# Performance work log

Hardware: AMD Instinct MI355X
Metric: run time of the kernel (lower is better)

## Reference

```python
import jax, jax.numpy as jnp
import numpy as np

N, D_IN, D_H, D_ATT, C_CLUST, N_CLS = 10000, 1024, 512, 256, 10, 4


def setup_inputs() -> dict:
    key = jax.random.key(0)
    ks = jax.random.split(key, 20)
    s = 0.02
    return {
        "x": jax.random.normal(ks[0], (N, D_IN), dtype=jnp.float32),
        "cluster_id": jax.random.randint(ks[1], (N,), 0, C_CLUST, dtype=jnp.int64),
        # per-cluster phi: Linear(1024->512) + ReLU + Linear(512->512) + ReLU
        "W1": s * jax.random.normal(ks[2], (C_CLUST, D_IN, D_H), dtype=jnp.float32),
        "b1": jnp.zeros((C_CLUST, D_H), dtype=jnp.float32),
        "W2": s * jax.random.normal(ks[3], (C_CLUST, D_H, D_H), dtype=jnp.float32),
        "b2": jnp.zeros((C_CLUST, D_H), dtype=jnp.float32),
        # attention_net fc: Linear(512->512)+ReLU
        "Wfc": s * jax.random.normal(ks[4], (D_H, D_H), dtype=jnp.float32),
        "bfc": jnp.zeros((D_H,), dtype=jnp.float32),
        # Attn_Net_Gated
        "Wa": s * jax.random.normal(ks[5], (D_H, D_ATT), dtype=jnp.float32),
        "ba": jnp.zeros((D_ATT,), dtype=jnp.float32),
        "Wb": s * jax.random.normal(ks[6], (D_H, D_ATT), dtype=jnp.float32),
        "bb": jnp.zeros((D_ATT,), dtype=jnp.float32),
        "Wc": s * jax.random.normal(ks[7], (D_ATT, 1), dtype=jnp.float32),
        "bc": jnp.zeros((1,), dtype=jnp.float32),
        # rho: Linear(512->256)+ReLU
        "Wr": s * jax.random.normal(ks[8], (D_H, D_ATT), dtype=jnp.float32),
        "br": jnp.zeros((D_ATT,), dtype=jnp.float32),
        # classifier: Linear(256->4)
        "Wcls": s * jax.random.normal(ks[9], (D_ATT, N_CLS), dtype=jnp.float32),
        "bcls": jnp.zeros((N_CLS,), dtype=jnp.float32),
    }


def reference(x, cluster_id, W1, b1, W2, b2, Wfc, bfc, Wa, ba, Wb, bb, Wc, bc, Wr, br, Wcls, bcls):
    C = W1.shape[0]
    # dense dispatch: apply every cluster's phi, then masked-mean per cluster
    # (ReLU is per-point elementwise, so masked mean == mean over members)
    h1 = jax.nn.relu(jnp.einsum('nd,cdh->cnh', x, W1) + b1[:, None, :])   # [C,N,512]
    h2 = jax.nn.relu(jnp.einsum('cnh,chk->cnk', h1, W2) + b2[:, None, :]) # [C,N,512]
    mask = (cluster_id[None, :] == jnp.arange(C)[:, None]).astype(h2.dtype)  # [C,N]
    counts = jnp.maximum(mask.sum(axis=1), 1.0)                           # [C]
    pooled = jnp.einsum('cnk,cn->ck', h2, mask) / counts[:, None]         # [C,512]
    # attention_net: fc + gated attention
    h = jax.nn.relu(pooled @ Wfc + bfc)                                   # [C,512]
    gate = jnp.tanh(h @ Wa + ba) * jax.nn.sigmoid(h @ Wb + bb)            # [C,256]
    A = (gate @ Wc + bc)                                                  # [C,1]
    A = jax.nn.softmax(A.T, axis=1)                                       # [1,C]
    h_path = A @ h                                                        # [1,512]
    hr = jax.nn.relu(h_path @ Wr + br)                                    # [1,256]
    logits = (hr[0] @ Wcls + bcls)[None, :]                               # [1,4]
    Y_prob = jax.nn.softmax(logits, axis=1)
    Y_hat = jnp.argmax(logits, axis=1)[:, None]
    return logits, Y_prob, Y_hat
```

## Files before the change

kernel.cpp:

```cpp
#include <hip/hip_runtime.h>
#include <math.h>

#define DIN 1024
#define DH 512
#define DATT 256
#define CNUM 10
#define NCLS 4
#define NH 64
#define NSC 40

typedef __attribute__((ext_vector_type(8))) short bf16x8;
typedef __attribute__((ext_vector_type(4))) float f32x4;
typedef unsigned short ushort_t;
typedef unsigned int uint_t;

__device__ inline ushort_t f2bf(float f) {
    uint_t u = __float_as_uint(f);
    u += 0x7FFF + ((u >> 16) & 1);
    return (ushort_t)(u >> 16);
}

__device__ inline void gl_lds16(const void* g, void* l) {
    __builtin_amdgcn_global_load_lds(
        (const __attribute__((address_space(1))) unsigned int*)g,
        (__attribute__((address_space(3))) unsigned int*)l, 16, 0, 0);
}


__global__ __launch_bounds__(256) void k_prep(
    const int* __restrict__ cid, int n, const float* __restrict__ bc,
    const float* __restrict__ x, const float* __restrict__ W1, const float* __restrict__ W2,
    ushort_t* __restrict__ xb, ushort_t* __restrict__ W1t, ushort_t* __restrict__ W2t,
    int nxb, int nw,
    float* __restrict__ a_logit, int* __restrict__ scat_pos, int* __restrict__ bucket)
{
    int bid = blockIdx.x;
    int t = threadIdx.x;

    if (bid == 0) {
        if (t < CNUM) a_logit[t] = bc[0];
        return;
    }
    bid -= 1;

    if (bid < NSC) {
        int lane = t & 63;
        for (int i = bid * 256 + t; i < n; i += NSC * 256) {
            int c = cid[i];
            #pragma unroll
            for (int cc = 0; cc < CNUM; cc++) {
                unsigned long long mask = __ballot(c == cc);
                if (mask == 0ull) continue;
                int leader = __ffsll(mask) - 1;
                int basep = 0;
                if (lane == leader) basep = atomicAdd(&scat_pos[cc], __popcll(mask));
                basep = __shfl(basep, leader, 64);
                if (c == cc) {
                    int rank = __popcll(mask & ((1ull << lane) - 1ull));
                    bucket[cc * n + basep + rank] = i;
                }
            }
        }
        return;
    }
    bid -= NSC;

    if (bid < nxb) {
        int row = bid * 4 + (t >> 6);
        if (row >= n) return;
        int col = (t & 63) * 16;
        const float* src = x + (size_t)row * DIN + col;
        ushort_t* dst = xb + (size_t)row * DIN + col;
        #pragma unroll
        for (int j = 0; j < 4; j++) {
            float4 v = *(const float4*)(src + 4 * j);
            *(ushort4*)(dst + 4 * j) = make_ushort4(f2bf(v.x), f2bf(v.y), f2bf(v.z), f2bf(v.w));
        }
        return;
    }
    bid -= nxb;

    if (bid < nw) {
        __shared__ float tile[64][65];
        int z = bid >> 7;
        int kx = (bid & 127) >> 3;
        int ny = bid & 7;
        const float* src; ushort_t* dst; int K;
        if (z < CNUM) { K = DIN; src = W1 + (size_t)z * K * DH; dst = W1t + (size_t)z * DH * K; }
        else          { K = DH;  src = W2 + (size_t)(z - CNUM) * K * DH; dst = W2t + (size_t)(z - CNUM) * DH * K; }
        int k0 = kx * 64;
        if (k0 >= K) return;
        int n0 = ny * 64;
        int rr = t >> 4;
        int cc = (t & 15) * 4;
        #pragma unroll
        for (int i = 0; i < 4; i++) {
            int row = rr + 16 * i;
            float4 v = *(const float4*)(src + (size_t)(k0 + row) * DH + n0 + cc);
            tile[row][cc + 0] = v.x; tile[row][cc + 1] = v.y;
            tile[row][cc + 2] = v.z; tile[row][cc + 3] = v.w;
        }
        __syncthreads();
        #pragma unroll
        for (int i = 0; i < 4; i++) {
            int nrow = rr + 16 * i;
            ushort4 o = make_ushort4(f2bf(tile[cc + 0][nrow]), f2bf(tile[cc + 1][nrow]),
                                     f2bf(tile[cc + 2][nrow]), f2bf(tile[cc + 3][nrow]));
            *(ushort4*)(dst + (size_t)(n0 + nrow) * K + k0 + cc) = o;
        }
    }
}


__device__ inline void stage4(
    const ushort_t* a0, const ushort_t* a1,
    const ushort_t* b0, const ushort_t* b1,
    int ko, ushort_t* As, ushort_t* Bs, int t)
{
    gl_lds16(a0 + ko, As + 0 * 2048 + t * 8);
    gl_lds16(a1 + ko, As + 1 * 2048 + t * 8);
    gl_lds16(b0 + ko, Bs + 0 * 2048 + t * 8);
    gl_lds16(b1 + ko, Bs + 1 * 2048 + t * 8);
}

__device__ inline void mfma_tile64(const ushort_t* As, const ushort_t* Bs,
                                   f32x4 (&acc)[2][2], int wr, int wc, int m, int quad)
{
    bf16x8 a[2][2], b[2][2];
    #pragma unroll
    for (int ks = 0; ks < 2; ks++) {
        int chunk = ((ks * 4 + quad) ^ (m & 7)) * 8;
        #pragma unroll
        for (int mf = 0; mf < 2; mf++)
            a[ks][mf] = *(const bf16x8*)(As + (32 * wr + 16 * mf + m) * 64 + chunk);
        #pragma unroll
        for (int nf = 0; nf < 2; nf++)
            b[ks][nf] = *(const bf16x8*)(Bs + (32 * wc + 16 * nf + m) * 64 + chunk);
    }
    asm volatile("s_waitcnt lgkmcnt(0)" ::: "memory");
    __builtin_amdgcn_sched_barrier(0);
    __builtin_amdgcn_s_barrier();
    __builtin_amdgcn_sched_barrier(0);
    #pragma unroll
    for (int ks = 0; ks < 2; ks++)
        #pragma unroll
        for (int mf = 0; mf < 2; mf++)
            #pragma unroll
            for (int nf = 0; nf < 2; nf++)
                acc[mf][nf] = __builtin_amdgcn_mfma_f32_16x16x32_bf16(a[ks][mf], b[ks][nf], acc[mf][nf], 0, 0, 0);
}

__device__ inline void gemm_loop64(
    const ushort_t* a0, const ushort_t* a1,
    const ushort_t* b0, const ushort_t* b1,
    int KT, f32x4 (&acc)[2][2], ushort_t* As, ushort_t* Bs)
{
    int t = threadIdx.x;
    int lane = t & 63;
    int w = t >> 6, wr = w >> 1, wc = w & 1;
    int m = lane & 15, quad = lane >> 4;

    stage4(a0, a1, b0, b1, 0, As, Bs, t);
    for (int kt = 0; kt < KT; kt += 2) {
        stage4(a0, a1, b0, b1, (kt + 1) * 64, As + 4096, Bs + 4096, t);
        asm volatile("s_waitcnt vmcnt(4)" ::: "memory");
        __builtin_amdgcn_sched_barrier(0);
        __builtin_amdgcn_s_barrier();
        __builtin_amdgcn_sched_barrier(0);
        mfma_tile64(As, Bs, acc, wr, wc, m, quad);

        if (kt + 2 < KT) {
            stage4(a0, a1, b0, b1, (kt + 2) * 64, As, Bs, t);
            asm volatile("s_waitcnt vmcnt(4)" ::: "memory");
        } else {
            asm volatile("s_waitcnt vmcnt(0)" ::: "memory");
        }
        __builtin_amdgcn_sched_barrier(0);
        __builtin_amdgcn_s_barrier();
        __builtin_amdgcn_sched_barrier(0);
        mfma_tile64(As + 4096, Bs + 4096, acc, wr, wc, m, quad);
    }
}

__device__ inline int tile_decode(int bid, int MAXT, const int* counts,
                                  int& c, int& m0, int& tile_n)
{
    int mt, nt;
    if ((MAXT & 7) == 0) {
        int mtpx = MAXT >> 3;
        int xcd = bid & 7, j = bid >> 3;
        nt = j / mtpx;
        mt = xcd * mtpx + (j - nt * mtpx);
    } else { mt = bid >> 3; nt = bid & 7; }

    int rem = mt;
    c = 0;
    #pragma unroll
    for (int cc = 0; cc < CNUM; cc++) {
        int tc = (counts[cc] + 63) >> 6;
        if (rem < tc) { c = cc; m0 = rem * 64; tile_n = nt * 64; return 1; }
        rem -= tc;
    }
    return 0;
}

__global__ __launch_bounds__(256, 4) void k_g1(
    const ushort_t* __restrict__ xb, const ushort_t* __restrict__ W1t,
    const float* __restrict__ b1, const int* __restrict__ bucket,
    const int* __restrict__ counts, int n, int MAXT,
    ushort_t* __restrict__ H1)
{
    __shared__ ushort_t As[2][64][64];
    __shared__ ushort_t Bs[2][64][64];

    int c, m0, tile_n;
    if (!tile_decode(blockIdx.x, MAXT, counts, c, m0, tile_n)) return;
    int cnt = counts[c];

    int t = threadIdx.x;
    int rr = t >> 3;
    int swz = ((t & 7) ^ (rr & 7)) * 8;

    const ushort_t* aP[2];
    const ushort_t* bP[2];
    #pragma unroll
    for (int s = 0; s < 2; s++) {
        int ra = m0 + s * 32 + rr;
        if (ra > cnt - 1) ra = cnt - 1;
        aP[s] = xb + (size_t)bucket[c * n + ra] * DIN + swz;
        bP[s] = W1t + ((size_t)c * DH + tile_n + s * 32 + rr) * DIN + swz;
    }

    f32x4 acc[2][2] = {};
    gemm_loop64(aP[0], aP[1], bP[0], bP[1], DIN / 64, acc, &As[0][0][0], &Bs[0][0][0]);

    int lane = t & 63;
    int w = t >> 6, wr = w >> 1, wc = w & 1;
    int m = lane & 15, quad = lane >> 4;
    int col0 = tile_n + 32 * wc;
    #pragma unroll
    for (int nf = 0; nf < 2; nf++) {
        int col = col0 + 16 * nf + m;
        float bv = b1[c * DH + col];
        #pragma unroll
        for (int mf = 0; mf < 2; mf++) {
            int rowb = m0 + 32 * wr + 16 * mf + quad * 4;
            #pragma unroll
            for (int r = 0; r < 4; r++) {
                int row = rowb + r;
                if (row < cnt)
                    H1[((size_t)c * n + row) * DH + col] = f2bf(fmaxf(acc[mf][nf][r] + bv, 0.f));
            }
        }
    }
}

__global__ __launch_bounds__(256, 4) void k_g2(
    const ushort_t* __restrict__ H1, const ushort_t* __restrict__ W2t,
    const float* __restrict__ b2, const int* __restrict__ counts, int n, int MAXT,
    float* __restrict__ pooled)
{
    __shared__ ushort_t As[2][64][64];
    __shared__ ushort_t Bs[2][64][64];

    int c, m0, tile_n;
    if (!tile_decode(blockIdx.x, MAXT, counts, c, m0, tile_n)) return;
    int cnt = counts[c];

    int t = threadIdx.x;
    int rr = t >> 3;
    int swz = ((t & 7) ^ (rr & 7)) * 8;

    const ushort_t* aP[2];
    const ushort_t* bP[2];
    #pragma unroll
    for (int s = 0; s < 2; s++) {
        int ra = m0 + s * 32 + rr;
        if (ra > cnt - 1) ra = cnt - 1;
        aP[s] = H1 + ((size_t)c * n + ra) * DH + swz;
        bP[s] = W2t + ((size_t)c * DH + tile_n + s * 32 + rr) * DH + swz;
    }

    f32x4 acc[2][2] = {};
    gemm_loop64(aP[0], aP[1], bP[0], bP[1], DH / 64, acc, &As[0][0][0], &Bs[0][0][0]);

    int lane = t & 63;
    int w = t >> 6, wr = w >> 1, wc = w & 1;
    int m = lane & 15, quad = lane >> 4;
    int col0 = tile_n + 32 * wc;
    #pragma unroll
    for (int nf = 0; nf < 2; nf++) {
        int col = col0 + 16 * nf + m;
        float bv = b2[c * DH + col];
        float s = 0.f;
        #pragma unroll
        for (int mf = 0; mf < 2; mf++) {
            int rowb = m0 + 32 * wr + 16 * mf + quad * 4;
            #pragma unroll
            for (int r = 0; r < 4; r++) {
                int row = rowb + r;
                if (row < cnt) s += fmaxf(acc[mf][nf][r] + bv, 0.f);
            }
        }
        s += __shfl_xor(s, 16);
        s += __shfl_xor(s, 32);
        if (quad == 0) atomicAdd(&pooled[c * DH + col], s);
    }
}


__global__ __launch_bounds__(256) void k_fc2(
    const float* __restrict__ pooled, const int* __restrict__ counts,
    const float* __restrict__ Wfc, const float* __restrict__ bfc,
    float* __restrict__ hfc)
{
    int c = blockIdx.x;
    int c0 = blockIdx.y * 64;
    __shared__ float ps[DH];
    __shared__ float red[4][64];
    int t = threadIdx.x;
    float cnt = fmaxf((float)counts[c], 1.f);
    ps[t] = pooled[c * DH + t] / cnt;
    ps[t + 256] = pooled[c * DH + t + 256] / cnt;
    __syncthreads();
    int col = c0 + (t & 63);
    int ks = t >> 6;
    float acc = 0.f;
    #pragma unroll 8
    for (int k = ks * 128; k < ks * 128 + 128; k++)
        acc = fmaf(ps[k], Wfc[(size_t)k * DH + col], acc);
    red[ks][t & 63] = acc;
    __syncthreads();
    if (t < 64) {
        float v = red[0][t] + red[1][t] + red[2][t] + red[3][t] + bfc[c0 + t];
        hfc[c * DH + c0 + t] = fmaxf(v, 0.f);
    }
}

__global__ __launch_bounds__(256) void k_gate2(
    const float* __restrict__ hfc,
    const float* __restrict__ Wa, const float* __restrict__ ba,
    const float* __restrict__ Wb, const float* __restrict__ bb,
    const float* __restrict__ Wc,
    float* __restrict__ a_logit)
{
    int c = blockIdx.x;
    int d0 = blockIdx.y * 64;
    __shared__ float hf[DH];
    __shared__ float ra[4][64], rb[4][64];
    int t = threadIdx.x;
    hf[t] = hfc[c * DH + t];
    hf[t + 256] = hfc[c * DH + t + 256];
    __syncthreads();
    int d = d0 + (t & 63);
    int ks = t >> 6;
    float ga = 0.f, gb = 0.f;
    #pragma unroll 8
    for (int k = ks * 128; k < ks * 128 + 128; k++) {
        float h = hf[k];
        ga = fmaf(h, Wa[(size_t)k * DATT + d], ga);
        gb = fmaf(h, Wb[(size_t)k * DATT + d], gb);
    }
    ra[ks][t & 63] = ga;
    rb[ks][t & 63] = gb;
    __syncthreads();
    if (t < 64) {
        float sa = ra[0][t] + ra[1][t] + ra[2][t] + ra[3][t] + ba[d0 + t];
        float sb = rb[0][t] + rb[1][t] + rb[2][t] + rb[3][t] + bb[d0 + t];
        float g = tanhf(sa) * (1.f / (1.f + expf(-sb)));
        float p = g * Wc[d0 + t];
        #pragma unroll
        for (int off = 32; off >= 1; off >>= 1) p += __shfl_down(p, off, 64);
        if (t == 0) atomicAdd(&a_logit[c], p);
    }
}

__global__ __launch_bounds__(1024) void k_final(
    const float* __restrict__ hfc, const float* __restrict__ a_logit,
    const float* __restrict__ Wr, const float* __restrict__ br,
    const float* __restrict__ Wcls, const float* __restrict__ bcls,
    float* __restrict__ out)
{
    int t = threadIdx.x;
    __shared__ float hp[DH];
    __shared__ float r1[4][DATT];
    __shared__ float hr[DATT];
    __shared__ float wred[4][NCLS];

    float al[CNUM];
    float m = -1e30f;
    #pragma unroll
    for (int c = 0; c < CNUM; c++) { al[c] = a_logit[c]; m = fmaxf(m, al[c]); }
    float s = 0.f;
    #pragma unroll
    for (int c = 0; c < CNUM; c++) { al[c] = expf(al[c] - m); s += al[c]; }
    float inv = 1.f / s;

    if (t < DH) {
        float v = 0.f;
        #pragma unroll
        for (int c = 0; c < CNUM; c++) v = fmaf(al[c] * inv, hfc[c * DH + t], v);
        hp[t] = v;
    }
    __syncthreads();

    int d = t & 255;
    int ks = t >> 8;
    float acc = 0.f;
    #pragma unroll 8
    for (int k = ks * 128; k < ks * 128 + 128; k++)
        acc = fmaf(hp[k], Wr[(size_t)k * DATT + d], acc);
    r1[ks][d] = acc;
    __syncthreads();
    if (t < DATT)
        hr[t] = fmaxf(r1[0][t] + r1[1][t] + r1[2][t] + r1[3][t] + br[t], 0.f);
    __syncthreads();

    if (t < 256) {
        float h = hr[t];
        #pragma unroll
        for (int cls = 0; cls < NCLS; cls++) {
            float p = h * Wcls[(size_t)t * NCLS + cls];
            #pragma unroll
            for (int off = 32; off >= 1; off >>= 1) p += __shfl_down(p, off, 64);
            if ((t & 63) == 0) wred[t >> 6][cls] = p;
        }
    }
// ... 44 lines not shown
            }
        }
        __syncthreads();
        if (t < CNUM) counts_part[bid * 16 + t] = h[t];
        return;
    }

    for (int i = t; i < CNUM * DH; i += 256) pooled[i] = 0.f;
    if (t < CNUM) a_logit[t] = bc[0];
    if (t < CNUM) scat_pos[t] = 0;
}

__global__ __launch_bounds__(256) void k_scat_fb(
    const int* __restrict__ cid, int n, const int* __restrict__ counts_part,
    int* __restrict__ counts, int* __restrict__ offsets,
    int* __restrict__ scat_pos, int* __restrict__ bucket)
{
    int bid = blockIdx.x;
    int t = threadIdx.x;
    __shared__ int cnts[CNUM], off[CNUM];
    if (t < CNUM) {
        int s = 0;
        #pragma unroll 8
        for (int b = 0; b < NH; b++) s += counts_part[b * 16 + t];
        cnts[t] = s;
    }
    __syncthreads();
    if (t == 0) {
        int a = 0;
        for (int c = 0; c < CNUM; c++) { off[c] = a; a += cnts[c]; }
        if (bid == 0) {
            int aa = 0;
            for (int c = 0; c < CNUM; c++) { offsets[c] = aa; counts[c] = cnts[c]; aa += cnts[c]; }
            offsets[CNUM] = aa;
        }
    }
    __syncthreads();
    int lane = t & 63;
    for (int i = bid * 256 + t; i < n; i += NSC * 256) {
        int c = cid[i];
        #pragma unroll
        for (int cc = 0; cc < CNUM; cc++) {
            unsigned long long mask = __ballot(c == cc);
            if (mask == 0ull) continue;
            int leader = __ffsll(mask) - 1;
            int basep = 0;
            if (lane == leader) basep = atomicAdd(&scat_pos[cc], __popcll(mask));
            basep = __shfl(basep, leader, 64);
            if (c == cc) {
                int rank = __popcll(mask & ((1ull << lane) - 1ull));
                bucket[off[cc] + basep + rank] = i;
            }
        }
    }
}

#define MT 64
#define NT 128
#define KT 32

__global__ __launch_bounds__(256) void k_gemm1(
    const float* __restrict__ x, const float* __restrict__ W1, const float* __restrict__ b1,
    const int* __restrict__ bucket, const int* __restrict__ offsets, const int* __restrict__ counts,
    float* __restrict__ H1)
{
    int c = blockIdx.z;
    int cnt = counts[c];
    int m0 = blockIdx.x * MT;
    if (m0 >= cnt) return;
    int rows = min(MT, cnt - m0);
    int n0 = blockIdx.y * NT;
    int base = offsets[c];

    __shared__ float As[KT][MT + 4];
    __shared__ float Bs[KT][NT];

    int t = threadIdx.x;
    int tr = t >> 4;
    int tc = t & 15;
    int lr = t >> 2;
    int lk = (t & 3) * 8;
    const float* xrow = nullptr;
    if (lr < rows) xrow = x + (size_t)bucket[base + m0 + lr] * DIN;

    float acc[4][8];
    #pragma unroll
    for (int i = 0; i < 4; i++)
        #pragma unroll
        for (int j = 0; j < 8; j++) acc[i][j] = 0.f;

    const float* Wp = W1 + (size_t)c * DIN * DH + n0;

    for (int k0 = 0; k0 < DIN; k0 += KT) {
        __syncthreads();
        if (xrow) {
            float4 v0 = *(const float4*)(xrow + k0 + lk);
            float4 v1 = *(const float4*)(xrow + k0 + lk + 4);
            As[lk + 0][lr] = v0.x; As[lk + 1][lr] = v0.y;
            As[lk + 2][lr] = v0.z; As[lk + 3][lr] = v0.w;
            As[lk + 4][lr] = v1.x; As[lk + 5][lr] = v1.y;
            As[lk + 6][lr] = v1.z; As[lk + 7][lr] = v1.w;
        } else {
            #pragma unroll
            for (int i = 0; i < 8; i++) As[lk + i][lr] = 0.f;
        }
        #pragma unroll
// ... 111 lines not shown
        float s = 0.f;
        #pragma unroll
        for (int i = 0; i < 4; i++) {
            if (4 * tr + i < rows) s += fmaxf(acc[i][j] + bias, 0.f);
        }
        red[tr][cidx] = s;
    }
    __syncthreads();
    if (t < NT) {
        float s = 0.f;
        #pragma unroll
        for (int r = 0; r < 16; r++) s += red[r][t];
        atomicAdd(&pooled[c * DH + n0 + t], s);
    }
}


extern "C" void kernel_launch(void* const* d_in, const int* in_sizes, int n_in,
                              void* d_out, int out_size, void* d_ws, size_t ws_size,
                              hipStream_t stream) {
    (void)n_in; (void)out_size;
    const float* x    = (const float*)d_in[0];
    const int*   cid  = (const int*)d_in[1];
    const float* W1   = (const float*)d_in[2];
    const float* b1   = (const float*)d_in[3];
    const float* W2   = (const float*)d_in[4];
    const float* b2   = (const float*)d_in[5];
    const float* Wfc  = (const float*)d_in[6];
    const float* bfc  = (const float*)d_in[7];
    const float* Wa   = (const float*)d_in[8];
    const float* ba   = (const float*)d_in[9];
    const float* Wb   = (const float*)d_in[10];
    const float* bb   = (const float*)d_in[11];
    const float* Wc   = (const float*)d_in[12];
    const float* bc   = (const float*)d_in[13];
    const float* Wr   = (const float*)d_in[14];
    const float* br   = (const float*)d_in[15];
    const float* Wcls = (const float*)d_in[16];
    const float* bcls = (const float*)d_in[17];
    float* out = (float*)d_out;
    float* ws  = (float*)d_ws;

    int n = in_sizes[1];

    float* pooled   = ws;
    int*   scat_pos = (int*)(ws + 5120);
    float* a_logit  = ws + 5136;
    float* hfc      = ws + 5152;
    int*   bucket   = (int*)(ws + 10272);

    size_t big0 = (((size_t)(10272 + (size_t)CNUM * n) * 4) + 255) & ~(size_t)255;
    size_t w1t_bytes = (size_t)CNUM * DH * DIN * 2;
    size_t w2t_bytes = (size_t)CNUM * DH * DH * 2;
    size_t h1_bytes  = (size_t)CNUM * n * DH * 2;
    size_t xb_bytes  = (size_t)n * DIN * 2;
    size_t need = big0 + w1t_bytes + w2t_bytes + h1_bytes + xb_bytes;

    if (ws_size >= need) {
        ushort_t* W1t = (ushort_t*)((char*)d_ws + big0);
        ushort_t* W2t = (ushort_t*)((char*)d_ws + big0 + w1t_bytes);
        ushort_t* H1  = (ushort_t*)((char*)d_ws + big0 + w1t_bytes + w2t_bytes);
        ushort_t* xb  = (ushort_t*)((char*)d_ws + big0 + w1t_bytes + w2t_bytes + h1_bytes);

        int nxb = (n + 3) / 4;
        int nw  = 128 * 2 * CNUM;
        int MAXT = ((n / 64 + CNUM + 1) + 7) & ~7;

        hipMemsetAsync(ws, 0, 5136 * 4, stream);
        k_prep<<<1 + NSC + nxb + nw, 256, 0, stream>>>(
            cid, n, bc, x, W1, W2, xb, W1t, W2t, nxb, nw, a_logit, scat_pos, bucket);
        k_g1<<<8 * MAXT, 256, 0, stream>>>(xb, W1t, b1, bucket, scat_pos, n, MAXT, H1);
        k_g2<<<8 * MAXT, 256, 0, stream>>>(H1, W2t, b2, scat_pos, n, MAXT, pooled);
        k_fc2<<<dim3(CNUM, 8), 256, 0, stream>>>(pooled, scat_pos, Wfc, bfc, hfc);
        k_gate2<<<dim3(CNUM, 4), 256, 0, stream>>>(hfc, Wa, ba, Wb, bb, Wc, a_logit);
        k_final<<<1, 1024, 0, stream>>>(hfc, a_logit, Wr, br, Wcls, bcls, out);
    } else {
        float* pooledF     = ws + 0;
        int*   countsF     = (int*)(ws + 5120);
        int*   offsetsF    = (int*)(ws + 5136);
        float* a_logitF    = ws + 5168;
        int*   scat_posF   = (int*)(ws + 5184);
        float* hfcF        = ws + 5200;
        int*   counts_part = (int*)(ws + 10320);
        int*   bucketF     = (int*)(ws + 11344);

        k_hist<<<NH + 1, 256, 0, stream>>>(cid, n, bc, counts_part, pooledF, a_logitF, scat_posF);
        k_scat_fb<<<NSC, 256, 0, stream>>>(cid, n, counts_part, countsF, offsetsF, scat_posF, bucketF);

        float* H1f = ws + ((11344 + n + 31) & ~31);
        dim3 gg((n + MT - 1) / MT, DH / NT, CNUM);
        k_gemm1<<<gg, 256, 0, stream>>>(x, W1, b1, bucketF, offsetsF, countsF, H1f);
        k_gemm2<<<gg, 256, 0, stream>>>(H1f, W2, b2, offsetsF, countsF, pooledF);

        k_fc2<<<dim3(CNUM, 8), 256, 0, stream>>>(pooledF, countsF, Wfc, bfc, hfcF);
        k_gate2<<<dim3(CNUM, 4), 256, 0, stream>>>(hfcF, Wa, ba, Wb, bb, Wc, a_logitF);
        k_final<<<1, 1024, 0, stream>>>(hfcF, a_logitF, Wr, br, Wcls, bcls, out);
    }
}
```

Baseline: 221.7 us.

## Fuse x bf16 conversion into GEMM1 A-load and merge head kernels

Removes the separate pass that converts x to bf16. The first grouped GEMM now reads the fp32 rows of x gathered through the bucket, converts them in registers with packed bf16 converts and writes them to LDS, while W1 still streams through global-to-LDS loads. The fc and gated-attention kernels are merged into one 512-thread kernel per cluster that computes the attention logit directly, so the atomic and the bc initialisation go away. In exchange, GEMM1 fetches fp32 A data at twice the bytes, once per N tile (8 times per row), and uses a simpler double-buffered pipeline with extra barriers. The merged head kernel also runs fewer blocks.

Result: slower. 284.5 us (+28.4%).

```diff
diff --git a/kernel.cpp b/kernel.cpp
--- a/kernel.cpp
+++ b/kernel.cpp
@@ -20,6 +20,12 @@
     return (ushort_t)(u >> 16);
 }
 
+__device__ inline uint_t pkbf(float lo, float hi) {
+    uint_t r;
+    asm("v_cvt_pk_bf16_f32 %0, %1, %2" : "=v"(r) : "v"(lo), "v"(hi));
+    return r;
+}
+
 __device__ inline void gl_lds16(const void* g, void* l) {
     __builtin_amdgcn_global_load_lds(
         (const __attribute__((address_space(1))) unsigned int*)g,
@@ -28,20 +34,14 @@
 
 
 __global__ __launch_bounds__(256) void k_prep(
-    const int* __restrict__ cid, int n, const float* __restrict__ bc,
-    const float* __restrict__ x, const float* __restrict__ W1, const float* __restrict__ W2,
-    ushort_t* __restrict__ xb, ushort_t* __restrict__ W1t, ushort_t* __restrict__ W2t,
-    int nxb, int nw,
-    float* __restrict__ a_logit, int* __restrict__ scat_pos, int* __restrict__ bucket)
+    const int* __restrict__ cid, int n,
+    const float* __restrict__ W1, const float* __restrict__ W2,
+    ushort_t* __restrict__ W1t, ushort_t* __restrict__ W2t,
+    int nw,
+    int* __restrict__ scat_pos, int* __restrict__ bucket)
 {
     int bid = blockIdx.x;
     int t = threadIdx.x;
-
-    if (bid == 0) {
-        if (t < CNUM) a_logit[t] = bc[0];
-        return;
-    }
-    bid -= 1;
 
     if (bid < NSC) {
         int lane = t & 63;
@@ -64,21 +64,6 @@
         return;
     }
     bid -= NSC;
-
-    if (bid < nxb) {
-        int row = bid * 4 + (t >> 6);
-        if (row >= n) return;
-        int col = (t & 63) * 16;
-        const float* src = x + (size_t)row * DIN + col;
-        ushort_t* dst = xb + (size_t)row * DIN + col;
-        #pragma unroll
-        for (int j = 0; j < 4; j++) {
-            float4 v = *(const float4*)(src + 4 * j);
-            *(ushort4*)(dst + 4 * j) = make_ushort4(f2bf(v.x), f2bf(v.y), f2bf(v.z), f2bf(v.w));
-        }
-        return;
-    }
-    bid -= nxb;
 
     if (bid < nw) {
         __shared__ float tile[64][65];
@@ -112,6 +97,150 @@
 }
 
 
+__device__ inline void awrite(ushort_t* A, int o0, int o1,
+                              const float4& r0, const float4& r1,
+                              const float4& r2, const float4& r3)
+{
+    uint4 w0, w1;
+    w0.x = pkbf(r0.x, r0.y); w0.y = pkbf(r0.z, r0.w);
+    w0.z = pkbf(r1.x, r1.y); w0.w = pkbf(r1.z, r1.w);
+    w1.x = pkbf(r2.x, r2.y); w1.y = pkbf(r2.z, r2.w);
+    w1.z = pkbf(r3.x, r3.y); w1.w = pkbf(r3.z, r3.w);
+    *(uint4*)(A + o0) = w0;
+    *(uint4*)(A + o1) = w1;
+}
+
+__device__ inline int tile_decode(int bid, int MAXT, const int* counts,
+                                  int& c, int& m0, int& tile_n)
+{
+    int mt, nt;
+    if ((MAXT & 7) == 0) {
+        int mtpx = MAXT >> 3;
+        int xcd = bid & 7, j = bid >> 3;
+        nt = j / mtpx;
+        mt = xcd * mtpx + (j - nt * mtpx);
+    } else { mt = bid >> 3; nt = bid & 7; }
+
+    int rem = mt;
+    c = 0;
+    #pragma unroll
+    for (int cc = 0; cc < CNUM; cc++) {
+        int tc = (counts[cc] + 63) >> 6;
+        if (rem < tc) { c = cc; m0 = rem * 64; tile_n = nt * 64; return 1; }
+        rem -= tc;
+    }
+    return 0;
+}
+
+
+__global__ __launch_bounds__(256, 4) void k_g1(
+    const float* __restrict__ x, const ushort_t* __restrict__ W1t,
+    const float* __restrict__ b1, const int* __restrict__ bucket,
+    const int* __restrict__ counts, int n, int MAXT,
+    ushort_t* __restrict__ H1)
+{
+    __shared__ ushort_t As[2][64][64];
+    __shared__ ushort_t Bs[2][64][64];
+
+    int c, m0, tile_n;
+    if (!tile_decode(blockIdx.x, MAXT, counts, c, m0, tile_n)) return;
+    int cnt = counts[c];
+
+    int t = threadIdx.x;
+    int lane = t & 63;
+    int w = t >> 6, wr = w >> 1, wc = w & 1;
+    int m = lane & 15, quad = lane >> 4;
+
+    int ar = t >> 2;
+    int aseg = (t & 3) * 16;
+    int ga = m0 + ar; if (ga > cnt - 1) ga = cnt - 1;
+    const float* aSrc = x + (size_t)bucket[c * n + ga] * DIN + aseg;
+    int c0 = (t & 3) * 2;
+    int awo0 = ar * 64 + ((c0    ) ^ (ar & 7)) * 8;
+    int awo1 = ar * 64 + ((c0 + 1) ^ (ar & 7)) * 8;
+
+    int rb = t >> 3;
+    int swz = ((t & 7) ^ (rb & 7)) * 8;
+    const ushort_t* bSrc0 = W1t + ((size_t)c * DH + tile_n +  0 + rb) * DIN + swz;
+    const ushort_t* bSrc1 = W1t + ((size_t)c * DH + tile_n + 32 + rb) * DIN + swz;
+
+    f32x4 acc[2][2] = {};
+    float4 r0, r1, r2, r3;
+
+    r0 = *(const float4*)(aSrc + 0);  r1 = *(const float4*)(aSrc + 4);
+    r2 = *(const float4*)(aSrc + 8);  r3 = *(const float4*)(aSrc + 12);
+    gl_lds16(bSrc0, &Bs[0][0][0]  + t * 8);
+    gl_lds16(bSrc1, &Bs[0][32][0] + t * 8);
+    awrite(&As[0][0][0], awo0, awo1, r0, r1, r2, r3);
+    asm volatile("s_waitcnt lgkmcnt(0)" ::: "memory");
+    asm volatile("s_waitcnt vmcnt(0)" ::: "memory");
+
+    #pragma unroll 2
+    for (int kt = 0; kt < DIN / 64; kt++) {
+        int cur = kt & 1, nxt = cur ^ 1;
+        if (kt + 1 < DIN / 64) {
+            const float* ap = aSrc + (kt + 1) * 64;
+            r0 = *(const float4*)(ap + 0);  r1 = *(const float4*)(ap + 4);
+            r2 = *(const float4*)(ap + 8);  r3 = *(const float4*)(ap + 12);
+            gl_lds16(bSrc0 + (kt + 1) * 64, &Bs[nxt][0][0]  + t * 8);
+            gl_lds16(bSrc1 + (kt + 1) * 64, &Bs[nxt][32][0] + t * 8);
+            asm volatile("s_waitcnt vmcnt(6)" ::: "memory");
+        } else {
+            asm volatile("s_waitcnt vmcnt(0)" ::: "memory");
+        }
+        __builtin_amdgcn_sched_barrier(0);
+        __builtin_amdgcn_s_barrier();
+        __builtin_amdgcn_sched_barrier(0);
+
+        bf16x8 a[2][2], b[2][2];
+        #pragma unroll
+        for (int ks = 0; ks < 2; ks++) {
+            int chunk = ((ks * 4 + quad) ^ (m & 7)) * 8;
+            #pragma unroll
+            for (int mf = 0; mf < 2; mf++)
+                a[ks][mf] = *(const bf16x8*)(&As[cur][0][0] + (32 * wr + 16 * mf + m) * 64 + chunk);
+            #pragma unroll
+            for (int nf = 0; nf < 2; nf++)
+                b[ks][nf] = *(const bf16x8*)(&Bs[cur][0][0] + (32 * wc + 16 * nf + m) * 64 + chunk);
+        }
+        asm volatile("s_waitcnt lgkmcnt(0)" ::: "memory");
+        __builtin_amdgcn_sched_barrier(0);
+        __builtin_amdgcn_s_barrier();
+        __builtin_amdgcn_sched_barrier(0);
+
+        #pragma unroll
+        for (int ks = 0; ks < 2; ks++)
+            #pragma unroll
+            for (int mf = 0; mf < 2; mf++)
+                #pragma unroll
+                for (int nf = 0; nf < 2; nf++)
+                    acc[mf][nf] = __builtin_amdgcn_mfma_f32_16x16x32_bf16(a[ks][mf], b[ks][nf], acc[mf][nf], 0, 0, 0);
+
+        if (kt + 1 < DIN / 64) {
+            awrite(&As[nxt][0][0], awo0, awo1, r0, r1, r2, r3);
+            asm volatile("s_waitcnt lgkmcnt(0)" ::: "memory");
+        }
+    }
+
+    int col0 = tile_n + 32 * wc;
+    #pragma unroll
+    for (int nf = 0; nf < 2; nf++) {
+        int col = col0 + 16 * nf + m;
+        float bv = b1[c * DH + col];
+        #pragma unroll
+        for (int mf = 0; mf < 2; mf++) {
+            int rowb = m0 + 32 * wr + 16 * mf + quad * 4;
+            #pragma unroll
+            for (int r = 0; r < 4; r++) {
+                int row = rowb + r;
+                if (row < cnt)
+                    H1[((size_t)c * n + row) * DH + col] = f2bf(fmaxf(acc[mf][nf][r] + bv, 0.f));
+            }
+        }
+    }
+}
+
+
 __device__ inline void stage4(
     const ushort_t* a0, const ushort_t* a1,
     const ushort_t* b0, const ushort_t* b1,
@@ -182,79 +311,6 @@
     }
 }
 
-__device__ inline int tile_decode(int bid, int MAXT, const int* counts,
-                                  int& c, int& m0, int& tile_n)
-{
-    int mt, nt;
-    if ((MAXT & 7) == 0) {
-        int mtpx = MAXT >> 3;
-        int xcd = bid & 7, j = bid >> 3;
-        nt = j / mtpx;
-        mt = xcd * mtpx + (j - nt * mtpx);
-    } else { mt = bid >> 3; nt = bid & 7; }
-
-    int rem = mt;
-    c = 0;
-    #pragma unroll
-    for (int cc = 0; cc < CNUM; cc++) {
-        int tc = (counts[cc] + 63) >> 6;
-        if (rem < tc) { c = cc; m0 = rem * 64; tile_n = nt * 64; return 1; }
-        rem -= tc;
-    }
-    return 0;
-}
-
-__global__ __launch_bounds__(256, 4) void k_g1(
-    const ushort_t* __restrict__ xb, const ushort_t* __restrict__ W1t,
-    const float* __restrict__ b1, const int* __restrict__ bucket,
-    const int* __restrict__ counts, int n, int MAXT,
-    ushort_t* __restrict__ H1)
-{
-    __shared__ ushort_t As[2][64][64];
-    __shared__ ushort_t Bs[2][64][64];
-
-    int c, m0, tile_n;
-    if (!tile_decode(blockIdx.x, MAXT, counts, c, m0, tile_n)) return;
-    int cnt = counts[c];
-
-    int t = threadIdx.x;
-    int rr = t >> 3;
-    int swz = ((t & 7) ^ (rr & 7)) * 8;
-
-    const ushort_t* aP[2];
-    const ushort_t* bP[2];
-    #pragma unroll
-    for (int s = 0; s < 2; s++) {
-        int ra = m0 + s * 32 + rr;
-        if (ra > cnt - 1) ra = cnt - 1;
-        aP[s] = xb + (size_t)bucket[c * n + ra] * DIN + swz;
-        bP[s] = W1t + ((size_t)c * DH + tile_n + s * 32 + rr) * DIN + swz;
-    }
-
-    f32x4 acc[2][2] = {};
-    gemm_loop64(aP[0], aP[1], bP[0], bP[1], DIN / 64, acc, &As[0][0][0], &Bs[0][0][0]);
-
-    int lane = t & 63;
-    int w = t >> 6, wr = w >> 1, wc = w & 1;
-    int m = lane & 15, quad = lane >> 4;
-    int col0 = tile_n + 32 * wc;
-    #pragma unroll
-    for (int nf = 0; nf < 2; nf++) {
-        int col = col0 + 16 * nf + m;
-        float bv = b1[c * DH + col];
-        #pragma unroll
-        for (int mf = 0; mf < 2; mf++) {
-            int rowb = m0 + 32 * wr + 16 * mf + quad * 4;
-            #pragma unroll
-            for (int r = 0; r < 4; r++) {
-                int row = rowb + r;
-                if (row < cnt)
-                    H1[((size_t)c * n + row) * DH + col] = f2bf(fmaxf(acc[mf][nf][r] + bv, 0.f));
-            }
-        }
-    }
-}
-
 __global__ __launch_bounds__(256, 4) void k_g2(
     const ushort_t* __restrict__ H1, const ushort_t* __restrict__ W2t,
     const float* __restrict__ b2, const int* __restrict__ counts, int n, int MAXT,
@@ -309,70 +365,59 @@
 }
 
 
-__global__ __launch_bounds__(256) void k_fc2(
+__global__ __launch_bounds__(512) void k_head(
     const float* __restrict__ pooled, const int* __restrict__ counts,
     const float* __restrict__ Wfc, const float* __restrict__ bfc,
-    float* __restrict__ hfc)
+    const float* __restrict__ Wa, const float* __restrict__ ba,
+    const float* __restrict__ Wb, const float* __restrict__ bb,
+    const float* __restrict__ Wc, const float* __restrict__ bc,
+    float* __restrict__ hfc, float* __restrict__ a_logit)
 {
     int c = blockIdx.x;
-    int c0 = blockIdx.y * 64;
+    int t = threadIdx.x;
     __shared__ float ps[DH];
-    __shared__ float red[4][64];
-    int t = threadIdx.x;
+    __shared__ float hf[DH];
+    __shared__ float ra[2][DATT], rb[2][DATT];
+    __shared__ float wred[4];
+
     float cnt = fmaxf((float)counts[c], 1.f);
     ps[t] = pooled[c * DH + t] / cnt;
-    ps[t + 256] = pooled[c * DH + t + 256] / cnt;
-    __syncthreads();
-    int col = c0 + (t & 63);
-    int ks = t >> 6;
-    float acc = 0.f;
-    #pragma unroll 8
-    for (int k = ks * 128; k < ks * 128 + 128; k++)
-        acc = fmaf(ps[k], Wfc[(size_t)k * DH + col], acc);
-    red[ks][t & 63] = acc;
-    __syncthreads();
-    if (t < 64) {
-        float v = red[0][t] + red[1][t] + red[2][t] + red[3][t] + bfc[c0 + t];
-        hfc[c * DH + c0 + t] = fmaxf(v, 0.f);
-    }
-}
-
-__global__ __launch_bounds__(256) void k_gate2(
-    const float* __restrict__ hfc,
-    const float* __restrict__ Wa, const float* __restrict__ ba,
-    const float* __restrict__ Wb, const float* __restrict__ bb,
-    const float* __restrict__ Wc,
-    float* __restrict__ a_logit)
-{
-    int c = blockIdx.x;
-    int d0 = blockIdx.y * 64;
-    __shared__ float hf[DH];
-    __shared__ float ra[4][64], rb[4][64];
-    int t = threadIdx.x;
-    hf[t] = hfc[c * DH + t];
-    hf[t + 256] = hfc[c * DH + t + 256];
-    __syncthreads();
-    int d = d0 + (t & 63);
-    int ks = t >> 6;
+    __syncthreads();
+
+    float a0 = 0.f, a1 = 0.f;
+    #pragma unroll 4
+    for (int k = 0; k < DH; k += 2) {
+        a0 = fmaf(ps[k],     Wfc[(size_t)k * DH + t],       a0);
+        a1 = fmaf(ps[k + 1], Wfc[(size_t)(k + 1) * DH + t], a1);
+    }
+    float h = fmaxf(a0 + a1 + bfc[t], 0.f);
+    hf[t] = h;
+    hfc[c * DH + t] = h;
+    __syncthreads();
+
+    int d = t & 255, half = t >> 8;
     float ga = 0.f, gb = 0.f;
-    #pragma unroll 8
-    for (int k = ks * 128; k < ks * 128 + 128; k++) {
-        float h = hf[k];
-        ga = fmaf(h, Wa[(size_t)k * DATT + d], ga);
-        gb = fmaf(h, Wb[(size_t)k * DATT + d], gb);
-    }
-    ra[ks][t & 63] = ga;
-    rb[ks][t & 63] = gb;
-    __syncthreads();
-    if (t < 64) {
-        float sa = ra[0][t] + ra[1][t] + ra[2][t] + ra[3][t] + ba[d0 + t];
-        float sb = rb[0][t] + rb[1][t] + rb[2][t] + rb[3][t] + bb[d0 + t];
+    #pragma unroll 4
+    for (int k = half * 256; k < half * 256 + 256; k++) {
+        float hh = hf[k];
+        ga = fmaf(hh, Wa[(size_t)k * DATT + d], ga);
+        gb = fmaf(hh, Wb[(size_t)k * DATT + d], gb);
+    }
+    ra[half][d] = ga;
+    rb[half][d] = gb;
+    __syncthreads();
+
+    if (t < DATT) {
+        float sa = ra[0][t] + ra[1][t] + ba[t];
+        float sb = rb[0][t] + rb[1][t] + bb[t];
         float g = tanhf(sa) * (1.f / (1.f + expf(-sb)));
-        float p = g * Wc[d0 + t];
+        float p = g * Wc[t];
         #pragma unroll
         for (int off = 32; off >= 1; off >>= 1) p += __shfl_down(p, off, 64);
-        if (t == 0) atomicAdd(&a_logit[c], p);
-    }
+        if ((t & 63) == 0) wred[t >> 6] = p;
+    }
+    __syncthreads();
+    if (t == 0) a_logit[c] = bc[0] + wred[0] + wred[1] + wred[2] + wred[3];
 }
 
 __global__ __launch_bounds__(1024) void k_final(
@@ -523,6 +568,72 @@
                 bucket[off[cc] + basep + rank] = i;
             }
         }
+    }
+}
+
+__global__ __launch_bounds__(256) void k_fc2(
+    const float* __restrict__ pooled, const int* __restrict__ counts,
+    const float* __restrict__ Wfc, const float* __restrict__ bfc,
+    float* __restrict__ hfc)
+{
+    int c = blockIdx.x;
+    int c0 = blockIdx.y * 64;
+    __shared__ float ps[DH];
+    __shared__ float red[4][64];
+    int t = threadIdx.x;
+    float cnt = fmaxf((float)counts[c], 1.f);
+    ps[t] = pooled[c * DH + t] / cnt;
+    ps[t + 256] = pooled[c * DH + t + 256] / cnt;
+    __syncthreads();
+    int col = c0 + (t & 63);
+    int ks = t >> 6;
+    float acc = 0.f;
+    #pragma unroll 8
+    for (int k = ks * 128; k < ks * 128 + 128; k++)
+        acc = fmaf(ps[k], Wfc[(size_t)k * DH + col], acc);
+    red[ks][t & 63] = acc;
+    __syncthreads();
+    if (t < 64) {
+        float v = red[0][t] + red[1][t] + red[2][t] + red[3][t] + bfc[c0 + t];
+        hfc[c * DH + c0 + t] = fmaxf(v, 0.f);
+    }
+}
+
+__global__ __launch_bounds__(256) void k_gate2(
+    const float* __restrict__ hfc,
+    const float* __restrict__ Wa, const float* __restrict__ ba,
+    const float* __restrict__ Wb, const float* __restrict__ bb,
+    const float* __restrict__ Wc,
+    float* __restrict__ a_logit)
+{
+    int c = blockIdx.x;
+    int d0 = blockIdx.y * 64;
+    __shared__ float hf[DH];
+    __shared__ float ra[4][64], rb[4][64];
+    int t = threadIdx.x;
+    hf[t] = hfc[c * DH + t];
+    hf[t + 256] = hfc[c * DH + t + 256];
+    __syncthreads();
+    int d = d0 + (t & 63);
+    int ks = t >> 6;
+    float ga = 0.f, gb = 0.f;
+    #pragma unroll 8
+    for (int k = ks * 128; k < ks * 128 + 128; k++) {
+        float h = hf[k];
+        ga = fmaf(h, Wa[(size_t)k * DATT + d], ga);
+        gb = fmaf(h, Wb[(size_t)k * DATT + d], gb);
+    }
+    ra[ks][t & 63] = ga;
+    rb[ks][t & 63] = gb;
+    __syncthreads();
+    if (t < 64) {
+        float sa = ra[0][t] + ra[1][t] + ra[2][t] + ra[3][t] + ba[d0 + t];
+        float sb = rb[0][t] + rb[1][t] + rb[2][t] + rb[3][t] + bb[d0 + t];
+        float g = tanhf(sa) * (1.f / (1.f + expf(-sb)));
+        float p = g * Wc[d0 + t];
+        #pragma unroll
+        for (int off = 32; off >= 1; off >>= 1) p += __shfl_down(p, off, 64);
+        if (t == 0) atomicAdd(&a_logit[c], p);
     }
 }
 
@@ -741,26 +852,21 @@
     size_t w1t_bytes = (size_t)CNUM * DH * DIN * 2;
     size_t w2t_bytes = (size_t)CNUM * DH * DH * 2;
     size_t h1_bytes  = (size_t)CNUM * n * DH * 2;
-    size_t xb_bytes  = (size_t)n * DIN * 2;
-    size_t need = big0 + w1t_bytes + w2t_bytes + h1_bytes + xb_bytes;
+    size_t need = big0 + w1t_bytes + w2t_bytes + h1_bytes;
 
     if (ws_size >= need) {
         ushort_t* W1t = (ushort_t*)((char*)d_ws + big0);
         ushort_t* W2t = (ushort_t*)((char*)d_ws + big0 + w1t_bytes);
         ushort_t* H1  = (ushort_t*)((char*)d_ws + big0 + w1t_bytes + w2t_bytes);
-        ushort_t* xb  = (ushort_t*)((char*)d_ws + big0 + w1t_bytes + w2t_bytes + h1_bytes);
-
-        int nxb = (n + 3) / 4;
+
         int nw  = 128 * 2 * CNUM;
         int MAXT = ((n / 64 + CNUM + 1) + 7) & ~7;
 
         hipMemsetAsync(ws, 0, 5136 * 4, stream);
-        k_prep<<<1 + NSC + nxb + nw, 256, 0, stream>>>(
-            cid, n, bc, x, W1, W2, xb, W1t, W2t, nxb, nw, a_logit, scat_pos, bucket);
-        k_g1<<<8 * MAXT, 256, 0, stream>>>(xb, W1t, b1, bucket, scat_pos, n, MAXT, H1);
+        k_prep<<<NSC + nw, 256, 0, stream>>>(cid, n, W1, W2, W1t, W2t, nw, scat_pos, bucket);
+        k_g1<<<8 * MAXT, 256, 0, stream>>>(x, W1t, b1, bucket, scat_pos, n, MAXT, H1);
         k_g2<<<8 * MAXT, 256, 0, stream>>>(H1, W2t, b2, scat_pos, n, MAXT, pooled);
-        k_fc2<<<dim3(CNUM, 8), 256, 0, stream>>>(pooled, scat_pos, Wfc, bfc, hfc);
-        k_gate2<<<dim3(CNUM, 4), 256, 0, stream>>>(hfc, Wa, ba, Wb, bb, Wc, a_logit);
+        k_head<<<CNUM, 512, 0, stream>>>(pooled, scat_pos, Wfc, bfc, Wa, ba, Wb, bb, Wc, bc, hfc, a_logit);
         k_final<<<1, 1024, 0, stream>>>(hfc, a_logit, Wr, br, Wcls, bcls, out);
     } else {
         float* pooledF     = ws + 0;
```

## Use three-stage LDS ring in grouped GEMMs and compact H1 layout

Applied to the files above, without the earlier changes.

Replaces the double-buffered K loop in both grouped GEMM kernels with a triple-buffered ring that keeps two tile loads in flight while computing, and lowers launch bounds from 4 to 3 blocks per CU to make room for the extra shared memory. H1 is stored compactly by per-cluster tile base offset instead of a CNUM*n strided layout, which shrinks the workspace. The bias for the attention logit moves into k_gate2 so the prep kernel no longer needs an extra block, and the memset grows to zero a_logit. The trade is more LDS per block and lower occupancy in exchange for deeper prefetch.

After: 220.9 us, median of 2. About the same (-0.3%).

```diff
diff --git a/kernel.cpp b/kernel.cpp
--- a/kernel.cpp
+++ b/kernel.cpp
@@ -28,20 +28,14 @@
 
 
 __global__ __launch_bounds__(256) void k_prep(
-    const int* __restrict__ cid, int n, const float* __restrict__ bc,
+    const int* __restrict__ cid, int n,
     const float* __restrict__ x, const float* __restrict__ W1, const float* __restrict__ W2,
     ushort_t* __restrict__ xb, ushort_t* __restrict__ W1t, ushort_t* __restrict__ W2t,
     int nxb, int nw,
-    float* __restrict__ a_logit, int* __restrict__ scat_pos, int* __restrict__ bucket)
+    int* __restrict__ scat_pos, int* __restrict__ bucket)
 {
     int bid = blockIdx.x;
     int t = threadIdx.x;
-
-    if (bid == 0) {
-        if (t < CNUM) a_logit[t] = bc[0];
-        return;
-    }
-    bid -= 1;
 
     if (bid < NSC) {
         int lane = t & 63;
@@ -123,34 +117,7 @@
     gl_lds16(b1 + ko, Bs + 1 * 2048 + t * 8);
 }
 
-__device__ inline void mfma_tile64(const ushort_t* As, const ushort_t* Bs,
-                                   f32x4 (&acc)[2][2], int wr, int wc, int m, int quad)
-{
-    bf16x8 a[2][2], b[2][2];
-    #pragma unroll
-    for (int ks = 0; ks < 2; ks++) {
-        int chunk = ((ks * 4 + quad) ^ (m & 7)) * 8;
-        #pragma unroll
-        for (int mf = 0; mf < 2; mf++)
-            a[ks][mf] = *(const bf16x8*)(As + (32 * wr + 16 * mf + m) * 64 + chunk);
-        #pragma unroll
-        for (int nf = 0; nf < 2; nf++)
-            b[ks][nf] = *(const bf16x8*)(Bs + (32 * wc + 16 * nf + m) * 64 + chunk);
-    }
-    asm volatile("s_waitcnt lgkmcnt(0)" ::: "memory");
-    __builtin_amdgcn_sched_barrier(0);
-    __builtin_amdgcn_s_barrier();
-    __builtin_amdgcn_sched_barrier(0);
-    #pragma unroll
-    for (int ks = 0; ks < 2; ks++)
-        #pragma unroll
-        for (int mf = 0; mf < 2; mf++)
-            #pragma unroll
-            for (int nf = 0; nf < 2; nf++)
-                acc[mf][nf] = __builtin_amdgcn_mfma_f32_16x16x32_bf16(a[ks][mf], b[ks][nf], acc[mf][nf], 0, 0, 0);
-}
-
-__device__ inline void gemm_loop64(
+__device__ inline void gemm_ring(
     const ushort_t* a0, const ushort_t* a1,
     const ushort_t* b0, const ushort_t* b1,
     int KT, f32x4 (&acc)[2][2], ushort_t* As, ushort_t* Bs)
@@ -160,30 +127,56 @@
     int w = t >> 6, wr = w >> 1, wc = w & 1;
     int m = lane & 15, quad = lane >> 4;
 
-    stage4(a0, a1, b0, b1, 0, As, Bs, t);
-    for (int kt = 0; kt < KT; kt += 2) {
-        stage4(a0, a1, b0, b1, (kt + 1) * 64, As + 4096, Bs + 4096, t);
-        asm volatile("s_waitcnt vmcnt(4)" ::: "memory");
+    stage4(a0, a1, b0, b1, 0,  As,        Bs,        t);
+    stage4(a0, a1, b0, b1, 64, As + 4096, Bs + 4096, t);
+
+    int buf = 0;
+    for (int kt = 0; kt < KT; kt++) {
+        if (kt + 2 < KT) {
+            int nb = buf + 2; if (nb >= 3) nb -= 3;
+            stage4(a0, a1, b0, b1, (kt + 2) * 64, As + nb * 4096, Bs + nb * 4096, t);
+            asm volatile("s_waitcnt vmcnt(8)" ::: "memory");
+        } else if (kt + 1 < KT) {
+            asm volatile("s_waitcnt vmcnt(4)" ::: "memory");
+        } else {
+            asm volatile("s_waitcnt vmcnt(0)" ::: "memory");
+        }
         __builtin_amdgcn_sched_barrier(0);
         __builtin_amdgcn_s_barrier();
         __builtin_amdgcn_sched_barrier(0);
-        mfma_tile64(As, Bs, acc, wr, wc, m, quad);
-
-        if (kt + 2 < KT) {
-            stage4(a0, a1, b0, b1, (kt + 2) * 64, As, Bs, t);
-            asm volatile("s_waitcnt vmcnt(4)" ::: "memory");
-        } else {
-            asm volatile("s_waitcnt vmcnt(0)" ::: "memory");
-        }
+
+        const ushort_t* Ab = As + buf * 4096;
+        const ushort_t* Bb = Bs + buf * 4096;
+        bf16x8 a[2][2], b[2][2];
+        #pragma unroll
+        for (int ks = 0; ks < 2; ks++) {
+            int chunk = ((ks * 4 + quad) ^ (m & 7)) * 8;
+            #pragma unroll
+            for (int mf = 0; mf < 2; mf++)
+                a[ks][mf] = *(const bf16x8*)(Ab + (32 * wr + 16 * mf + m) * 64 + chunk);
+            #pragma unroll
+            for (int nf = 0; nf < 2; nf++)
+                b[ks][nf] = *(const bf16x8*)(Bb + (32 * wc + 16 * nf + m) * 64 + chunk);
+        }
+        asm volatile("s_waitcnt lgkmcnt(0)" ::: "memory");
         __builtin_amdgcn_sched_barrier(0);
         __builtin_amdgcn_s_barrier();
         __builtin_amdgcn_sched_barrier(0);
-        mfma_tile64(As + 4096, Bs + 4096, acc, wr, wc, m, quad);
+
+        #pragma unroll
+        for (int ks = 0; ks < 2; ks++)
+            #pragma unroll
+            for (int mf = 0; mf < 2; mf++)
+                #pragma unroll
+                for (int nf = 0; nf < 2; nf++)
+                    acc[mf][nf] = __builtin_amdgcn_mfma_f32_16x16x32_bf16(a[ks][mf], b[ks][nf], acc[mf][nf], 0, 0, 0);
+
+        buf = buf + 1; if (buf == 3) buf = 0;
     }
 }
 
 __device__ inline int tile_decode(int bid, int MAXT, const int* counts,
-                                  int& c, int& m0, int& tile_n)
+                                  int& c, int& m0, int& tile_n, int& base)
 {
     int mt, nt;
     if ((MAXT & 7) == 0) {
@@ -194,27 +187,28 @@
     } else { mt = bid >> 3; nt = bid & 7; }
 
     int rem = mt;
-    c = 0;
+    c = 0; base = 0;
     #pragma unroll
     for (int cc = 0; cc < CNUM; cc++) {
         int tc = (counts[cc] + 63) >> 6;
         if (rem < tc) { c = cc; m0 = rem * 64; tile_n = nt * 64; return 1; }
         rem -= tc;
+        base += tc * 64;
     }
     return 0;
 }
 
-__global__ __launch_bounds__(256, 4) void k_g1(
+__global__ __launch_bounds__(256, 3) void k_g1(
     const ushort_t* __restrict__ xb, const ushort_t* __restrict__ W1t,
     const float* __restrict__ b1, const int* __restrict__ bucket,
     const int* __restrict__ counts, int n, int MAXT,
     ushort_t* __restrict__ H1)
 {
-    __shared__ ushort_t As[2][64][64];
-    __shared__ ushort_t Bs[2][64][64];
-
-    int c, m0, tile_n;
-    if (!tile_decode(blockIdx.x, MAXT, counts, c, m0, tile_n)) return;
+    __shared__ ushort_t As[3][64][64];
+    __shared__ ushort_t Bs[3][64][64];
+
+    int c, m0, tile_n, base;
+    if (!tile_decode(blockIdx.x, MAXT, counts, c, m0, tile_n, base)) return;
     int cnt = counts[c];
 
     int t = threadIdx.x;
@@ -227,12 +221,13 @@
     for (int s = 0; s < 2; s++) {
         int ra = m0 + s * 32 + rr;
         if (ra > cnt - 1) ra = cnt - 1;
+        if (ra < 0) ra = 0;
         aP[s] = xb + (size_t)bucket[c * n + ra] * DIN + swz;
         bP[s] = W1t + ((size_t)c * DH + tile_n + s * 32 + rr) * DIN + swz;
     }
 
     f32x4 acc[2][2] = {};
-    gemm_loop64(aP[0], aP[1], bP[0], bP[1], DIN / 64, acc, &As[0][0][0], &Bs[0][0][0]);
+    gemm_ring(aP[0], aP[1], bP[0], bP[1], DIN / 64, acc, &As[0][0][0], &Bs[0][0][0]);
 
     int lane = t & 63;
     int w = t >> 6, wr = w >> 1, wc = w & 1;
@@ -249,22 +244,22 @@
             for (int r = 0; r < 4; r++) {
                 int row = rowb + r;
                 if (row < cnt)
-                    H1[((size_t)c * n + row) * DH + col] = f2bf(fmaxf(acc[mf][nf][r] + bv, 0.f));
+                    H1[(size_t)(base + row) * DH + col] = f2bf(fmaxf(acc[mf][nf][r] + bv, 0.f));
             }
         }
     }
 }
 
-__global__ __launch_bounds__(256, 4) void k_g2(
+__global__ __launch_bounds__(256, 3) void k_g2(
     const ushort_t* __restrict__ H1, const ushort_t* __restrict__ W2t,
     const float* __restrict__ b2, const int* __restrict__ counts, int n, int MAXT,
     float* __restrict__ pooled)
 {
-    __shared__ ushort_t As[2][64][64];
-    __shared__ ushort_t Bs[2][64][64];
-
-    int c, m0, tile_n;
-    if (!tile_decode(blockIdx.x, MAXT, counts, c, m0, tile_n)) return;
+    __shared__ ushort_t As[3][64][64];
+    __shared__ ushort_t Bs[3][64][64];
+
+    int c, m0, tile_n, base;
+    if (!tile_decode(blockIdx.x, MAXT, counts, c, m0, tile_n, base)) return;
     int cnt = counts[c];
 
     int t = threadIdx.x;
@@ -277,12 +272,13 @@
     for (int s = 0; s < 2; s++) {
         int ra = m0 + s * 32 + rr;
         if (ra > cnt - 1) ra = cnt - 1;
-        aP[s] = H1 + ((size_t)c * n + ra) * DH + swz;
+        if (ra < 0) ra = 0;
+        aP[s] = H1 + (size_t)(base + ra) * DH + swz;
         bP[s] = W2t + ((size_t)c * DH + tile_n + s * 32 + rr) * DH + swz;
     }
 
     f32x4 acc[2][2] = {};
-    gemm_loop64(aP[0], aP[1], bP[0], bP[1], DH / 64, acc, &As[0][0][0], &Bs[0][0][0]);
+    gemm_ring(aP[0], aP[1], bP[0], bP[1], DH / 64, acc, &As[0][0][0], &Bs[0][0][0]);
 
     int lane = t & 63;
     int w = t >> 6, wr = w >> 1, wc = w & 1;
@@ -341,7 +337,7 @@
     const float* __restrict__ hfc,
     const float* __restrict__ Wa, const float* __restrict__ ba,
     const float* __restrict__ Wb, const float* __restrict__ bb,
-    const float* __restrict__ Wc,
+    const float* __restrict__ Wc, const float* __restrict__ bc,
     float* __restrict__ a_logit)
 {
     int c = blockIdx.x;
@@ -371,7 +367,10 @@
         float p = g * Wc[d0 + t];
         #pragma unroll
         for (int off = 32; off >= 1; off >>= 1) p += __shfl_down(p, off, 64);
-        if (t == 0) atomicAdd(&a_logit[c], p);
+        if (t == 0) {
+            if (blockIdx.y == 0) p += bc[0];
+            atomicAdd(&a_logit[c], p);
+        }
     }
 }
 
@@ -523,6 +522,44 @@
                 bucket[off[cc] + basep + rank] = i;
             }
         }
+    }
+}
+
+__global__ __launch_bounds__(256) void k_gate2_fb(
+    const float* __restrict__ hfc,
+    const float* __restrict__ Wa, const float* __restrict__ ba,
+    const float* __restrict__ Wb, const float* __restrict__ bb,
+    const float* __restrict__ Wc,
+    float* __restrict__ a_logit)
+{
+    int c = blockIdx.x;
+    int d0 = blockIdx.y * 64;
+    __shared__ float hf[DH];
+    __shared__ float ra[4][64], rb[4][64];
+    int t = threadIdx.x;
+    hf[t] = hfc[c * DH + t];
+    hf[t + 256] = hfc[c * DH + t + 256];
+    __syncthreads();
+    int d = d0 + (t & 63);
+    int ks = t >> 6;
+    float ga = 0.f, gb = 0.f;
+    #pragma unroll 8
+    for (int k = ks * 128; k < ks * 128 + 128; k++) {
+        float h = hf[k];
+        ga = fmaf(h, Wa[(size_t)k * DATT + d], ga);
+        gb = fmaf(h, Wb[(size_t)k * DATT + d], gb);
+    }
+    ra[ks][t & 63] = ga;
+    rb[ks][t & 63] = gb;
+    __syncthreads();
+    if (t < 64) {
+        float sa = ra[0][t] + ra[1][t] + ra[2][t] + ra[3][t] + ba[d0 + t];
+        float sb = rb[0][t] + rb[1][t] + rb[2][t] + rb[3][t] + bb[d0 + t];
+        float g = tanhf(sa) * (1.f / (1.f + expf(-sb)));
+        float p = g * Wc[d0 + t];
+        #pragma unroll
+        for (int off = 32; off >= 1; off >>= 1) p += __shfl_down(p, off, 64);
+        if (t == 0) atomicAdd(&a_logit[c], p);
     }
 }
 
@@ -740,7 +777,7 @@
     size_t big0 = (((size_t)(10272 + (size_t)CNUM * n) * 4) + 255) & ~(size_t)255;
     size_t w1t_bytes = (size_t)CNUM * DH * DIN * 2;
     size_t w2t_bytes = (size_t)CNUM * DH * DH * 2;
-    size_t h1_bytes  = (size_t)CNUM * n * DH * 2;
+    size_t h1_bytes  = (size_t)(n + 64 * CNUM) * DH * 2;
     size_t xb_bytes  = (size_t)n * DIN * 2;
     size_t need = big0 + w1t_bytes + w2t_bytes + h1_bytes + xb_bytes;
 
@@ -754,13 +791,13 @@
         int nw  = 128 * 2 * CNUM;
         int MAXT = ((n / 64 + CNUM + 1) + 7) & ~7;
 
-        hipMemsetAsync(ws, 0, 5136 * 4, stream);
-        k_prep<<<1 + NSC + nxb + nw, 256, 0, stream>>>(
-            cid, n, bc, x, W1, W2, xb, W1t, W2t, nxb, nw, a_logit, scat_pos, bucket);
+        hipMemsetAsync(ws, 0, 5152 * 4, stream);
+        k_prep<<<NSC + nxb + nw, 256, 0, stream>>>(
+            cid, n, x, W1, W2, xb, W1t, W2t, nxb, nw, scat_pos, bucket);
         k_g1<<<8 * MAXT, 256, 0, stream>>>(xb, W1t, b1, bucket, scat_pos, n, MAXT, H1);
         k_g2<<<8 * MAXT, 256, 0, stream>>>(H1, W2t, b2, scat_pos, n, MAXT, pooled);
         k_fc2<<<dim3(CNUM, 8), 256, 0, stream>>>(pooled, scat_pos, Wfc, bfc, hfc);
-        k_gate2<<<dim3(CNUM, 4), 256, 0, stream>>>(hfc, Wa, ba, Wb, bb, Wc, a_logit);
+        k_gate2<<<dim3(CNUM, 4), 256, 0, stream>>>(hfc, Wa, ba, Wb, bb, Wc, bc, a_logit);
         k_final<<<1, 1024, 0, stream>>>(hfc, a_logit, Wr, br, Wcls, bcls, out);
     } else {
         float* pooledF     = ws + 0;
@@ -781,7 +818,7 @@
         k_gemm2<<<gg, 256, 0, stream>>>(H1f, W2, b2, offsetsF, countsF, pooledF);
 
         k_fc2<<<dim3(CNUM, 8), 256, 0, stream>>>(pooledF, countsF, Wfc, bfc, hfcF);
-        k_gate2<<<dim3(CNUM, 4), 256, 0, stream>>>(hfcF, Wa, ba, Wb, bb, Wc, a_logitF);
+        k_gate2_fb<<<dim3(CNUM, 4), 256, 0, stream>>>(hfcF, Wa, ba, Wb, bb, Wc, a_logitF);
         k_final<<<1, 1024, 0, stream>>>(hfcF, a_logitF, Wr, br, Wcls, bcls, out);
     }
 }
```
